# Optimization experiments

Hardware: AMD Instinct MI355X
Metric: run time of the kernel (lower is better)

Reference implementation:

```python
import jax, jax.numpy as jnp
import numpy as np

B, IN, HID, H = 8192, 1024, 2048, 8
UP = 2 * IN          # input_size * proj_factor
HS = HID // H        # head size = 256
EPS = 1e-5


def _blockdiag(x, w, b):
    # x: [B, UP] -> chunk into H blocks of UP//H, per-block linear to HID//H
    xb = x.reshape(B, H, UP // H)
    y = jnp.einsum('bhi,hio->bho', xb, w)
    return y.reshape(B, HID) + b


def setup_inputs() -> dict:
    key = jax.random.key(0)
    ks = jax.random.split(key, 20)
    rn = lambda k, s: jax.random.normal(k, s, jnp.float32)
    p = lambda k, *s: rn(k, s) * 0.02
    return dict(
        x=rn(ks[0], (B, IN)),
        h_prev=rn(ks[1], (B, HID)), c_prev=rn(ks[2], (B, HID)),
        n_prev=rn(ks[3], (B, HID)), m_prev=rn(ks[4], (B, HID)),
        ln_g=jnp.ones(IN), ln_b=jnp.zeros(IN),
        w_ul=p(ks[5], IN, UP), b_ul=jnp.zeros(UP),
        w_ur=p(ks[6], IN, HID), b_ur=jnp.zeros(HID),
        conv_w=p(ks[7], 4), conv_b=jnp.zeros(()),
        w_skip=p(ks[8], UP, HID), b_skip=jnp.zeros(HID),
        w_q=p(ks[9], H, UP // H, HID // H), b_q=jnp.zeros(HID),
        w_k=p(ks[10], H, UP // H, HID // H), b_k=jnp.zeros(HID),
        w_v=p(ks[11], H, UP // H, HID // H), b_v=jnp.zeros(HID),
        w_i=p(ks[12], UP, HID), b_i=jnp.zeros(HID),
        w_f=p(ks[13], UP, HID), b_f=jnp.zeros(HID),
        w_o=p(ks[14], UP, HID), b_o=jnp.zeros(HID),
        gn_g=jnp.ones(HID), gn_b=jnp.zeros(HID),
        w_down=p(ks[15], HID, IN), b_down=jnp.zeros(IN),
    )


def reference(x, h_prev, c_prev, n_prev, m_prev, ln_g, ln_b,
              w_ul, b_ul, w_ur, b_ur, conv_w, conv_b, w_skip, b_skip,
              w_q, b_q, w_k, b_k, w_v, b_v, w_i, b_i, w_f, b_f, w_o, b_o,
              gn_g, gn_b, w_down, b_down):
    # LayerNorm over features
    mu = x.mean(-1, keepdims=True)
    var = x.var(-1, keepdims=True)
    xn = (x - mu) * jax.lax.rsqrt(var + EPS) * ln_g + ln_b

    xul = xn @ w_ul + b_ul          # [B, UP]
    xur = xn @ w_ur + b_ur          # [B, HID]

    # causal conv1d (kernel 4, 1 channel) along the feature axis, left-pad 3
    xp = jnp.pad(xul, ((0, 0), (3, 0)))
    xc = conv_b + sum(conv_w[j] * xp[:, j:j + UP] for j in range(4))
    xc = jax.nn.silu(xc)            # [B, UP]

    x_skip = xc @ w_skip + b_skip

    q = _blockdiag(xc, w_q, b_q)
    k = _blockdiag(xc, w_k, b_k) / np.sqrt(HS).astype(np.float32)
    v = _blockdiag(xul, w_v, b_v)

    i_t = xc @ w_i + b_i
    f_t = xc @ w_f + b_f
    o = jax.nn.sigmoid(xul @ w_o + b_o)

    m_t = jnp.maximum(f_t + m_prev, i_t)
    i = jnp.exp(i_t - m_t)
    f = jnp.exp(f_t + m_prev - m_t)
    c_t = f * c_prev + i * (v * k)
    n_t = f * n_prev + i * k

    denom = jnp.max(jnp.abs(n_t.T @ q), axis=1)     # [HID]
    h_t = o * (c_t * q) / denom

    # GroupNorm on (N, C), groups = H
    hg = h_t.reshape(B, H, HID // H)
    gm = hg.mean(-1, keepdims=True)
    gv = hg.var(-1, keepdims=True)
    hn = ((hg - gm) * jax.lax.rsqrt(gv + EPS)).reshape(B, HID) * gn_g + gn_b

    out = (hn + x_skip) * jax.nn.silu(xur)
    return out @ w_down + b_down + x, h_t, c_t, n_t, m_t
```

## Files before the change

kernel.cpp:

```cpp
#include <hip/hip_runtime.h>
#include <stdint.h>

#define B_    8192
#define IN_   1024
#define HID_  2048
#define UP_   2048
#define H_    8
#define HS_   256
#define EPS_  1e-5f

typedef __bf16 bf16x8 __attribute__((ext_vector_type(8)));
typedef float f32x4 __attribute__((ext_vector_type(4)));
typedef unsigned short u16x4 __attribute__((ext_vector_type(4)));
typedef unsigned short u16x8 __attribute__((ext_vector_type(8)));

__device__ __forceinline__ unsigned short f2bf(float f) {
  union { float f; unsigned int u; } v; v.f = f;
  unsigned int u = v.u;
  unsigned int r = (u + 0x7fffu + ((u >> 16) & 1u)) >> 16;
  return (unsigned short)r;
}
__device__ __forceinline__ float bf2f(unsigned short h) {
  union { unsigned int u; float f; } v; v.u = ((unsigned int)h) << 16;
  return v.f;
}

__device__ __forceinline__ void gload_lds16(const void* g, void* l) {
  auto gp = reinterpret_cast<const uint32_t __attribute__((address_space(1)))*>(
      reinterpret_cast<uintptr_t>(g));
  auto lp = reinterpret_cast<uint32_t __attribute__((address_space(3)))*>(
      reinterpret_cast<uintptr_t>(l));
  __builtin_amdgcn_global_load_lds(gp, lp, 16, 0, 0);
}

template <typename OutT, bool HAS_ADD>
__global__ __launch_bounds__(512, 2) void gemm8p(
    const unsigned short* __restrict__ A, int lda, int a_zoff,
    const unsigned short* __restrict__ W, int ldw, int w_zoff,
    const float* __restrict__ bias, const float* __restrict__ bias2,
    int bias_zoff,
    OutT* __restrict__ C, OutT* __restrict__ C2, int ldc, int c_zoff,
    int c_split,
    const float* __restrict__ ADD, float scale, float scale2, int K)
{
  __shared__ char lds[163840];
  const int z = blockIdx.z;
  A += (size_t)z * a_zoff;
  W += (size_t)z * w_zoff;
  if (bias) bias += (size_t)z * bias_zoff;
  if (bias2) bias2 += (size_t)z * bias_zoff;

  const int nwg = gridDim.x * gridDim.y;
  const int orig = blockIdx.y * gridDim.x + blockIdx.x;
  const int q8 = nwg >> 3, r8 = nwg & 7;
  const int xcd = orig & 7, xi = orig >> 3;
  const int wg = (xcd < r8 ? xcd * (q8 + 1) : r8 * (q8 + 1) + (xcd - r8) * q8) + xi;
  const int bx = wg % gridDim.x, by = wg / gridDim.x;

  const int t = threadIdx.x;
  const int lane = t & 63, wave = t >> 6;
  const int wr = wave >> 2, wc = wave & 3;
  const int l15 = lane & 15, l4 = lane >> 4;
  const int row0 = by * 256, col0 = bx * 256;

  const int lrow = lane >> 3;
  const int lslot = (lane & 7) ^ lrow;
  const size_t aLane = (size_t)lrow * lda * 2 + (size_t)lslot * 16;
  const size_t wLane = (size_t)lrow * ldw * 2 + (size_t)lslot * 16;
  const char* Abase = (const char*)A;
  const char* Wbase = (const char*)W;

  const int aRdBase = (wr * 128 + l15) * 128 + (((l4) ^ (l15 & 7)) * 16);
  const int bRdBase = (wc * 64 + l15) * 128 + (((l4) ^ (l15 & 7)) * 16);

  auto issueA = [&](int abuf, int half, int tile) {
#pragma unroll
    for (int j = 0; j < 2; ++j) {
      const int rbase = half * 128 + j * 64 + wave * 8;
      gload_lds16(Abase + (size_t)(row0 + rbase) * (lda * 2) + (size_t)tile * 128 + aLane,
                  lds + abuf * 32768 + rbase * 128 + lane * 16);
    }
  };
  auto issueB = [&](int bbuf, int half, int tile) {
#pragma unroll
    for (int j = 0; j < 2; ++j) {
      const int rbase = half * 128 + j * 64 + wave * 8;
      gload_lds16(Wbase + (size_t)(col0 + rbase) * (ldw * 2) + (size_t)tile * 128 + wLane,
                  lds + 98304 + bbuf * 32768 + rbase * 128 + lane * 16);
    }
  };

  f32x4 acc[8][4] = {};
  const int NT = K >> 6;

  issueA(0, 0, 0); issueA(0, 1, 0);
  issueB(0, 0, 0); issueB(0, 1, 0);
  if (NT > 1) {
    issueA(1, 0, 1); issueA(1, 1, 1);
    issueB(1, 0, 1); issueB(1, 1, 1);
    asm volatile("s_waitcnt vmcnt(8)" ::: "memory");
  } else {
    asm volatile("s_waitcnt vmcnt(0)" ::: "memory");
  }
  __builtin_amdgcn_s_barrier();
  __builtin_amdgcn_sched_barrier(0);

  for (int T = 0; T < NT; ++T) {
    const char* ldsA = lds + (T % 3) * 32768;
    const char* ldsB = lds + 98304 + (T & 1) * 32768;
    const int abufN = (T + 2) % 3;
    const int bbufN = T & 1;
    bf16x8 bfr[4][2];
#pragma unroll
    for (int q = 0; q < 4; ++q) {
      if (q == 0) {
#pragma unroll
        for (int ni = 0; ni < 4; ++ni) {
          bfr[ni][0] = *(const bf16x8*)(ldsB + (bRdBase + ni * 2048));
          bfr[ni][1] = *(const bf16x8*)(ldsB + ((bRdBase + ni * 2048) ^ 64));
        }
      }
      bf16x8 af[2][2];
#pragma unroll
      for (int m2 = 0; m2 < 2; ++m2) {
        const int mi = q * 2 + m2;
        af[m2][0] = *(const bf16x8*)(ldsA + (aRdBase + mi * 2048));
        af[m2][1] = *(const bf16x8*)(ldsA + ((aRdBase + mi * 2048) ^ 64));
      }
      if (q == 0 && T + 2 < NT) issueA(abufN, 0, T + 2);
      if (q == 1 && T + 2 < NT) issueA(abufN, 1, T + 2);
      if (q == 2 && T + 2 < NT) issueB(bbufN, 0, T + 2);
      if (q == 3 && T + 2 < NT) issueB(bbufN, 1, T + 2);
      if (q == 0) asm volatile("s_waitcnt lgkmcnt(8)" ::: "memory");
      __builtin_amdgcn_s_barrier();
      asm volatile("s_waitcnt lgkmcnt(0)" ::: "memory");
      __builtin_amdgcn_sched_barrier(0);
      __builtin_amdgcn_s_setprio(1);
#pragma unroll
      for (int kq = 0; kq < 2; ++kq)
#pragma unroll
        for (int m2 = 0; m2 < 2; ++m2)
#pragma unroll
          for (int ni = 0; ni < 4; ++ni)
            acc[q * 2 + m2][ni] = __builtin_amdgcn_mfma_f32_16x16x32_bf16(
                af[m2][kq], bfr[ni][kq], acc[q * 2 + m2][ni], 0, 0, 0);
      __builtin_amdgcn_s_setprio(0);
      if (q == 3) {
        if (T + 2 < NT) asm volatile("s_waitcnt vmcnt(8)" ::: "memory");
        else            asm volatile("s_waitcnt vmcnt(0)" ::: "memory");
      }
      __builtin_amdgcn_s_barrier();
      __builtin_amdgcn_sched_barrier(0);
    }
  }

  const float* bp = bias;
  OutT* Cp = C;
  int cbase = col0;
  float sc = scale;
  if (col0 >= c_split) { bp = bias2; Cp = C2; cbase = col0 - c_split; sc = scale2; }
#pragma unroll
  for (int mi = 0; mi < 8; ++mi) {
#pragma unroll
    for (int ni = 0; ni < 4; ++ni) {
#pragma unroll
      for (int r = 0; r < 4; ++r) {
        const int m = row0 + wr * 128 + mi * 16 + l4 * 4 + r;
        const int n = wc * 64 + ni * 16 + l15;
        float v = acc[mi][ni][r];
        if (bp) v += bp[cbase + n];
        v *= sc;
        const size_t ci = (size_t)m * ldc + (size_t)z * c_zoff + cbase + n;
        if constexpr (HAS_ADD) v += ADD[ci];
        if constexpr (sizeof(OutT) == 2) Cp[ci] = (OutT)f2bf(v);
        else Cp[ci] = v;
      }
    }
  }
}

__global__ __launch_bounds__(256) void denom_reduce(
    const float* __restrict__ part, float* __restrict__ denom)
{
  const int m = blockIdx.x, t = threadIdx.x;
  const size_t P = (size_t)HID_ * HID_;
  float v = 0.f;
  for (int n = t; n < HID_; n += 256) {
    const size_t o = (size_t)m * HID_ + n;
    float s = part[o] + part[P + o] + part[2 * P + o] + part[3 * P + o];
    v = fmaxf(v, fabsf(s));
  }
#pragma unroll
  for (int off = 1; off < 64; off <<= 1) v = fmaxf(v, __shfl_xor(v, off, 64));
  __shared__ float red[4];
  if ((t & 63) == 0) red[t >> 6] = v;
  __syncthreads();
  if (t == 0) denom[m] = fmaxf(fmaxf(red[0], red[1]), fmaxf(red[2], red[3]));
}

__global__ __launch_bounds__(256) void down_reduce(
    const float* __restrict__ part, const float* __restrict__ x,
    const float* __restrict__ bias, float* __restrict__ out)
{
  const size_t idx = ((size_t)blockIdx.x * 256 + threadIdx.x) * 4;
  const size_t P = (size_t)B_ * IN_;
  f32x4 a = *(const f32x4*)(part + idx);
  f32x4 b = *(const f32x4*)(part + P + idx);
  f32x4 xv = *(const f32x4*)(x + idx);
  const int j = (int)(idx & (IN_ - 1));
  f32x4 bv = *(const f32x4*)(bias + j);
  f32x4 o;
#pragma unroll
  for (int e = 0; e < 4; ++e) o[e] = a[e] + b[e] + bv[e] + xv[e];
  *(f32x4*)(out + idx) = o;
}

template <typename InT>
__global__ __launch_bounds__(256) void transpose_bf(
    const InT* __restrict__ in, unsigned short* __restrict__ out, int R, int C,
    int izoff, int ozoff)
{
  __shared__ float tile[32][33];
  in += (size_t)blockIdx.z * izoff;
  out += (size_t)blockIdx.z * ozoff;
  const int cb = blockIdx.x * 32, rb = blockIdx.y * 32;
  const int tx = threadIdx.x, ty = threadIdx.y;
  for (int i = ty; i < 32; i += 8) {
    InT v = in[(size_t)(rb + i) * C + cb + tx];
    float f;
    if constexpr (sizeof(InT) == 2) f = bf2f((unsigned short)v);
    else f = (float)v;
    tile[i][tx] = f;
  }
  __syncthreads();
  for (int i = ty; i < 32; i += 8)
    out[(size_t)(cb + i) * R + rb + tx] = f2bf(tile[tx][i]);
}

__global__ __launch_bounds__(256) void ln_kernel(
    const float* __restrict__ x, const float* __restrict__ g,
    const float* __restrict__ b, unsigned short* __restrict__ xn)
{
  const int brow = blockIdx.x, t = threadIdx.x;
  const int lane = t & 63, wave = t >> 6;
  const float* xr = x + (size_t)brow * IN_;
  f32x4 v = *(const f32x4*)(xr + t * 4);
  float s = v[0] + v[1] + v[2] + v[3];
  float q = v[0]*v[0] + v[1]*v[1] + v[2]*v[2] + v[3]*v[3];
#pragma unroll
  for (int off = 32; off; off >>= 1) {
    s += __shfl_xor(s, off, 64);
    q += __shfl_xor(q, off, 64);
  }
  __shared__ float ss[4], sq[4];
  if (lane == 0) { ss[wave] = s; sq[wave] = q; }
  __syncthreads();
  s = ss[0] + ss[1] + ss[2] + ss[3];
  q = sq[0] + sq[1] + sq[2] + sq[3];
  const float mean = s * (1.f / IN_);
  const float var = q * (1.f / IN_) - mean * mean;
  const float rs = rsqrtf(var + EPS_);
  u16x4 o;
#pragma unroll
  for (int e = 0; e < 4; ++e) {
    const int j = t * 4 + e;
    o[e] = f2bf((v[e] - mean) * rs * g[j] + b[j]);
  }
  *(u16x4*)(xn + (size_t)brow * IN_ + t * 4) = o;
}

__global__ __launch_bounds__(256) void conv_kernel(
    const unsigned short* __restrict__ xul, const float* __restrict__ cw,
    const float* __restrict__ cb, unsigned short* __restrict__ xc)
{
  const int brow = blockIdx.x, t = threadIdx.x;
  const size_t base = (size_t)brow * UP_;
  const int j0 = t * 8;
  float xv[11];
#pragma unroll
  for (int e = 0; e < 11; ++e) {
    const int j = j0 + e - 3;
    xv[e] = (j >= 0) ? bf2f(xul[base + j]) : 0.f;
  }
  const float w0 = cw[0], w1 = cw[1], w2 = cw[2], w3 = cw[3], bb = cb[0];
  u16x8 o;
#pragma unroll
  for (int e = 0; e < 8; ++e) {
    float sv = bb + w0 * xv[e] + w1 * xv[e + 1] + w2 * xv[e + 2] + w3 * xv[e + 3];
    o[e] = f2bf(sv / (1.f + expf(-sv)));
  }
  *(u16x8*)(xc + base + j0) = o;
}

__global__ __launch_bounds__(256) void gates_kernel(
    const unsigned short* __restrict__ sif,
    const unsigned short* __restrict__ kb, const unsigned short* __restrict__ vb,
    const float* __restrict__ mprev, const float* __restrict__ cprev,
    const float* __restrict__ nprev,
    float* __restrict__ mo, float* __restrict__ co, float* __restrict__ no,
    unsigned short* __restrict__ nT)
{
  __shared__ unsigned short nt_t[64][72];
  const int t = threadIdx.x;
  const int r = t >> 2, cq = t & 3;
  const int row = blockIdx.y * 64 + r;
  const int colb = blockIdx.x * 64 + cq * 16;
  const size_t hidb = (size_t)row * HID_ + colb;
  const size_t sifb = (size_t)row * 6144 + colb;
#pragma unroll
  for (int e4 = 0; e4 < 4; ++e4) {
    const int c4 = e4 * 4;
    f32x4 mp = *(const f32x4*)(mprev + hidb + c4);
    f32x4 cp = *(const f32x4*)(cprev + hidb + c4);
    f32x4 np = *(const f32x4*)(nprev + hidb + c4);
    u16x4 iv = *(const u16x4*)(sif + sifb + 2048 + c4);
    u16x4 fv = *(const u16x4*)(sif + sifb + 4096 + c4);
    u16x4 kv = *(const u16x4*)(kb + hidb + c4);
    u16x4 vv = *(const u16x4*)(vb + hidb + c4);
    f32x4 mo4, co4, no4;
#pragma unroll
    for (int e = 0; e < 4; ++e) {
      const float ft = bf2f(fv[e]) + mp[e];
      const float it = bf2f(iv[e]);
      const float mt = fmaxf(ft, it);
      const float ie = expf(it - mt);
      const float fe = expf(ft - mt);
      const float k = bf2f(kv[e]), v = bf2f(vv[e]);
      mo4[e] = mt;
      co4[e] = fe * cp[e] + ie * (v * k);
      no4[e] = fe * np[e] + ie * k;
      nt_t[r][cq * 16 + c4 + e] = f2bf(no4[e]);
    }
    *(f32x4*)(mo + hidb + c4) = mo4;
    *(f32x4*)(co + hidb + c4) = co4;
    *(f32x4*)(no + hidb + c4) = no4;
  }
  __syncthreads();
  const int cT = t >> 2, sq = t & 3;
  u16x8 o0, o1;
#pragma unroll
  for (int e = 0; e < 8; ++e) {
    o0[e] = nt_t[sq * 16 + e][cT];
    o1[e] = nt_t[sq * 16 + 8 + e][cT];
  }
  const size_t ob = (size_t)(blockIdx.x * 64 + cT) * B_ + blockIdx.y * 64 + sq * 16;
  *(u16x8*)(nT + ob) = o0;
  *(u16x8*)(nT + ob + 8) = o1;
}

__global__ __launch_bounds__(256) void hgn_kernel(
    const float* __restrict__ ct, const unsigned short* __restrict__ olin,
    const unsigned short* __restrict__ qb, const float* __restrict__ denom,
    const unsigned short* __restrict__ sif, const unsigned short* __restrict__ xurb,
    const float* __restrict__ gng, const float* __restrict__ gnb,
    float* __restrict__ ho, unsigned short* __restrict__ pre)
{
  const int brow = blockIdx.x, t = threadIdx.x;
  const size_t base = (size_t)brow * HID_ + t * 8;
  u16x8 ov = *(const u16x8*)(olin + base);
  u16x8 qv = *(const u16x8*)(qb + base);
  f32x4 c0 = *(const f32x4*)(ct + base);
  f32x4 c1 = *(const f32x4*)(ct + base + 4);
  float h[8];
  float s = 0.f, sq = 0.f;
#pragma unroll
  for (int e = 0; e < 8; ++e) {
    const float o = 1.f / (1.f + expf(-bf2f(ov[e])));
    const float cv = (e < 4) ? c0[e] : c1[e - 4];
    const float hv = o * cv * bf2f(qv[e]) / denom[t * 8 + e];
    h[e] = hv; s += hv; sq += hv * hv;
  }
#pragma unroll
  for (int e = 0; e < 8; ++e) ho[base + e] = h[e];
#pragma unroll
  for (int off = 1; off < 32; off <<= 1) {
    s += __shfl_xor(s, off, 64);
    sq += __shfl_xor(sq, off, 64);
  }
  const float mean = s * (1.f / HS_);
  const float var = sq * (1.f / HS_) - mean * mean;
  const float rs = rsqrtf(var + EPS_);
  u16x8 sv = *(const u16x8*)(sif + (size_t)brow * 6144 + t * 8);
  u16x8 xv = *(const u16x8*)(xurb + base);
  u16x8 pv;
#pragma unroll
  for (int e = 0; e < 8; ++e) {
    const int j = t * 8 + e;
    const float hn = (h[e] - mean) * rs * gng[j] + gnb[j];
    const float xr = bf2f(xv[e]);
    const float sil = xr / (1.f + expf(-xr));
    pv[e] = f2bf((hn + bf2f(sv[e])) * sil);
  }
  *(u16x8*)(pre + base) = pv;
}

extern "C" void kernel_launch(void* const* d_in, const int* in_sizes, int n_in,
                              void* d_out, int out_size, void* d_ws, size_t ws_size,
                              hipStream_t stream)
{
  const float* x      = (const float*)d_in[0];
  const float* c_prev = (const float*)d_in[2];
  const float* n_prev = (const float*)d_in[3];
  const float* m_prev = (const float*)d_in[4];
  const float* ln_g   = (const float*)d_in[5];
  const float* ln_b   = (const float*)d_in[6];
  const float* w_ul   = (const float*)d_in[7];
  const float* b_ul   = (const float*)d_in[8];
  const float* w_ur   = (const float*)d_in[9];
  const float* b_ur   = (const float*)d_in[10];
  const float* conv_w = (const float*)d_in[11];
  const float* conv_b = (const float*)d_in[12];
  const float* w_skip = (const float*)d_in[13];
  const float* b_skip = (const float*)d_in[14];
  const float* w_q    = (const float*)d_in[15];
  const float* b_q    = (const float*)d_in[16];
  const float* w_k    = (const float*)d_in[17];
  const float* b_k    = (const float*)d_in[18];
  const float* w_v    = (const float*)d_in[19];
  const float* b_v    = (const float*)d_in[20];
  const float* w_i    = (const float*)d_in[21];
  const float* b_i    = (const float*)d_in[22];
  const float* w_f    = (const float*)d_in[23];
  const float* b_f    = (const float*)d_in[24];
  const float* w_o    = (const float*)d_in[25];
  const float* b_o    = (const float*)d_in[26];
  const float* gn_g   = (const float*)d_in[27];
  const float* gn_b   = (const float*)d_in[28];
  const float* w_down = (const float*)d_in[29];
  const float* b_down = (const float*)d_in[30];

  float* out_p = (float*)d_out;
  float* h_p = out_p + (size_t)B_ * IN_;
  float* c_p = h_p + (size_t)B_ * HID_;
  float* n_p = c_p + (size_t)B_ * HID_;
  float* m_p = n_p + (size_t)B_ * HID_;

  char* ws = (char*)d_ws;
  size_t off = 0;
  auto alloc = [&](size_t n) -> void* {
    void* p = ws + off;
    off += (n + 255) & ~(size_t)255;
    return p;
  };

  const size_t BH2 = (size_t)B_ * HID_ * 2;

  unsigned short* xn_bf   = (unsigned short*)alloc((size_t)B_ * IN_ * 2);
  unsigned short* xul_bf  = (unsigned short*)alloc(BH2);
  unsigned short* xur_bf  = (unsigned short*)alloc(BH2);
  unsigned short* xc_bf   = (unsigned short*)alloc(BH2);
  unsigned short* sif_bf  = (unsigned short*)alloc((size_t)B_ * 6144 * 2);
  unsigned short* q_bf    = (unsigned short*)alloc(BH2);
  unsigned short* k_bf    = (unsigned short*)alloc(BH2);
  unsigned short* v_bf    = (unsigned short*)alloc(BH2);
  unsigned short* olin_bf = (unsigned short*)alloc(BH2);
  unsigned short* qT_bf   = (unsigned short*)alloc(BH2);
  unsigned short* nT_bf   = (unsigned short*)alloc(BH2);
  unsigned short* pre_bf  = (unsigned short*)alloc(BH2);
  float* denom = (float*)alloc(HID_ * sizeof(float));
  float* part  = (float*)alloc((size_t)4 * HID_ * HID_ * sizeof(float));
  float* b_sif = (float*)alloc(6144 * sizeof(float));
  unsigned short* wt_ulur = (unsigned short*)alloc((size_t)4096 * IN_ * 2);
  unsigned short* wt_sif  = (unsigned short*)alloc((size_t)6144 * UP_ * 2);
  unsigned short* wt_qk   = (unsigned short*)alloc((size_t)H_ * 512 * HS_ * 2);
  unsigned short* wt_v    = (unsigned short*)alloc((size_t)H_ * HS_ * HS_ * 2);
  unsigned short* wt_o    = (unsigned short*)alloc((size_t)UP_ * HID_ * 2);
  unsigned short* wt_down = (unsigned short*)alloc((size_t)HID_ * IN_ * 2);

  if (off > ws_size) return;

  const dim3 tb32(32, 8);
  const int NOSPLIT = 1 << 30;

  hipMemcpyAsync(b_sif, b_skip, 2048 * 4, hipMemcpyDeviceToDevice, stream);
  hipMemcpyAsync(b_sif + 2048, b_i, 2048 * 4, hipMemcpyDeviceToDevice, stream);
  hipMemcpyAsync(b_sif + 4096, b_f, 2048 * 4, hipMemcpyDeviceToDevice, stream);

  transpose_bf<float><<<dim3(64, 32, 1), tb32, 0, stream>>>(w_ul, wt_ulur, 1024, 2048, 0, 0);
  transpose_bf<float><<<dim3(64, 32, 1), tb32, 0, stream>>>(w_ur, wt_ulur + (size_t)2048 * 1024, 1024, 2048, 0, 0);
  transpose_bf<float><<<dim3(64, 64, 1), tb32, 0, stream>>>(w_skip, wt_sif, 2048, 2048, 0, 0);
  transpose_bf<float><<<dim3(64, 64, 1), tb32, 0, stream>>>(w_i, wt_sif + (size_t)2048 * 2048, 2048, 2048, 0, 0);
  transpose_bf<float><<<dim3(64, 64, 1), tb32, 0, stream>>>(w_f, wt_sif + (size_t)4096 * 2048, 2048, 2048, 0, 0);
  transpose_bf<float><<<dim3(8, 8, 8), tb32, 0, stream>>>(w_q, wt_qk, 256, 256, 65536, 131072);
  transpose_bf<float><<<dim3(8, 8, 8), tb32, 0, stream>>>(w_k, wt_qk + 65536, 256, 256, 65536, 131072);
  transpose_bf<float><<<dim3(8, 8, 8), tb32, 0, stream>>>(w_v, wt_v, 256, 256, 65536, 65536);
  transpose_bf<float><<<dim3(64, 64, 1), tb32, 0, stream>>>(w_o, wt_o, 2048, 2048, 0, 0);
  transpose_bf<float><<<dim3(32, 64, 1), tb32, 0, stream>>>(w_down, wt_down, 2048, 1024, 0, 0);

  ln_kernel<<<B_, 256, 0, stream>>>(x, ln_g, ln_b, xn_bf);

  gemm8p<unsigned short, false><<<dim3(16, 32, 1), 512, 0, stream>>>(
      xn_bf, IN_, 0, wt_ulur, IN_, 0, b_ul, b_ur, 0,
      xul_bf, xur_bf, HID_, 0, 2048, nullptr, 1.f, 1.f, IN_);

  conv_kernel<<<B_, 256, 0, stream>>>(xul_bf, conv_w, conv_b, xc_bf);

  gemm8p<unsigned short, false><<<dim3(24, 32, 1), 512, 0, stream>>>(
      xc_bf, UP_, 0, wt_sif, UP_, 0, b_sif, nullptr, 0,
      sif_bf, sif_bf, 6144, 0, NOSPLIT, nullptr, 1.f, 1.f, UP_);

  gemm8p<unsigned short, false><<<dim3(2, 32, 8), 512, 0, stream>>>(
      xc_bf, UP_, HS_, wt_qk, HS_, 512 * HS_, b_q, b_k, HS_,
      q_bf, k_bf, HID_, HS_, 256, nullptr, 1.f, 0.0625f, HS_);

  gemm8p<unsigned short, false><<<dim3(1, 32, 8), 512, 0, stream>>>(
      xul_bf, UP_, HS_, wt_v, HS_, HS_ * HS_, b_v, nullptr, HS_,
      v_bf, v_bf, HID_, HS_, NOSPLIT, nullptr, 1.f, 1.f, HS_);

  gemm8p<unsigned short, false><<<dim3(8, 32, 1), 512, 0, stream>>>(
      xul_bf, UP_, 0, wt_o, UP_, 0, b_o, nullptr, 0,
      olin_bf, olin_bf, HID_, 0, NOSPLIT, nullptr, 1.f, 1.f, UP_);

  gates_kernel<<<dim3(HID_ / 64, B_ / 64, 1), 256, 0, stream>>>(
      sif_bf, k_bf, v_bf, m_prev, c_prev, n_prev, m_p, c_p, n_p, nT_bf);

  transpose_bf<unsigned short><<<dim3(64, 256, 1), tb32, 0, stream>>>(
      q_bf, qT_bf, B_, HID_, 0, 0);

  gemm8p<float, false><<<dim3(8, 8, 4), 512, 0, stream>>>(
      nT_bf, B_, B_ / 4, qT_bf, B_, B_ / 4, nullptr, nullptr, 0,
      part, part, HID_, HID_ * HID_, NOSPLIT, nullptr, 1.f, 1.f, B_ / 4);
  denom_reduce<<<HID_, 256, 0, stream>>>(part, denom);

  hgn_kernel<<<B_, 256, 0, stream>>>(
      c_p, olin_bf, q_bf, denom, sif_bf, xur_bf, gn_g, gn_b, h_p, pre_bf);

  gemm8p<float, false><<<dim3(4, 32, 2), 512, 0, stream>>>(
      pre_bf, UP_, 1024, wt_down, UP_, 1024, nullptr, nullptr, 0,
      part, part, IN_, B_ * IN_, NOSPLIT, nullptr, 1.f, 1.f, 1024);
  down_reduce<<<(B_ * IN_ / 4) / 256, 256, 0, stream>>>(part, x, b_down, out_p);
}
```

Baseline: 1.005 ms.

## Double-buffer A fragments in registers to overlap LDS reads with MFMA

Software-pipelines the LDS reads of the A-operand fragments in the GEMM main loop. Each quarter-step now runs its MFMA cluster on fragments loaded one step earlier, alternating between two register sets, and the last quarter prefetches the next K-tile's first fragments. The global-to-LDS issue, the vmcnt wait (now vmcnt(6)) and the barrier are moved ahead of the LDS reads so the next buffer is ready before it is prefetched. The aim is to hide LDS latency behind matrix math, at the cost of extra VGPRs under a 512-thread, 2-blocks-per-CU launch bound, which could cause spills.

```diff
diff --git a/kernel.cpp b/kernel.cpp
--- a/kernel.cpp
+++ b/kernel.cpp
@@ -32,6 +32,22 @@
       reinterpret_cast<uintptr_t>(l));
   __builtin_amdgcn_global_load_lds(gp, lp, 16, 0, 0);
 }
+
+#define PREFETCH_AF(DST, BASE, MI0)                                         \
+  DST[0][0] = *(const bf16x8*)((BASE) + (aRdBase + (MI0) * 2048));          \
+  DST[0][1] = *(const bf16x8*)((BASE) + ((aRdBase + (MI0) * 2048) ^ 64));   \
+  DST[1][0] = *(const bf16x8*)((BASE) + (aRdBase + ((MI0) + 1) * 2048));    \
+  DST[1][1] = *(const bf16x8*)((BASE) + ((aRdBase + ((MI0) + 1) * 2048) ^ 64));
+
+#define MFMA_CLUSTER(AF, Q)                                                 \
+  _Pragma("unroll")                                                         \
+  for (int kq = 0; kq < 2; ++kq)                                            \
+    _Pragma("unroll")                                                       \
+    for (int m2 = 0; m2 < 2; ++m2)                                          \
+      _Pragma("unroll")                                                     \
+      for (int ni = 0; ni < 4; ++ni)                                        \
+        acc[(Q) * 2 + m2][ni] = __builtin_amdgcn_mfma_f32_16x16x32_bf16(    \
+            AF[m2][kq], bfr[ni][kq], acc[(Q) * 2 + m2][ni], 0, 0, 0);
 
 template <typename OutT, bool HAS_ADD>
 __global__ __launch_bounds__(512, 2) void gemm8p(
@@ -93,6 +109,9 @@
   f32x4 acc[8][4] = {};
   const int NT = K >> 6;
 
+  bf16x8 bfr[4][2];
+  bf16x8 afA[2][2], afB[2][2];
+
   issueA(0, 0, 0); issueA(0, 1, 0);
   issueB(0, 0, 0); issueB(0, 1, 0);
   if (NT > 1) {
@@ -104,15 +123,28 @@
   }
   __builtin_amdgcn_s_barrier();
   __builtin_amdgcn_sched_barrier(0);
+  {
+    const char* ldsA0 = lds;
+    PREFETCH_AF(afA, ldsA0, 0)
+  }
 
   for (int T = 0; T < NT; ++T) {
     const char* ldsA = lds + (T % 3) * 32768;
+    const char* ldsAn = lds + ((T + 1) % 3) * 32768;
     const char* ldsB = lds + 98304 + (T & 1) * 32768;
     const int abufN = (T + 2) % 3;
     const int bbufN = T & 1;
-    bf16x8 bfr[4][2];
 #pragma unroll
     for (int q = 0; q < 4; ++q) {
+      if (q == 3) {
+        if (T + 2 < NT) asm volatile("s_waitcnt vmcnt(6)" ::: "memory");
+        else            asm volatile("s_waitcnt vmcnt(0)" ::: "memory");
+      }
+      if (q == 0 && T + 2 < NT) issueA(abufN, 0, T + 2);
+      if (q == 1 && T + 2 < NT) issueA(abufN, 1, T + 2);
+      if (q == 2 && T + 2 < NT) issueB(bbufN, 0, T + 2);
+      if (q == 3 && T + 2 < NT) issueB(bbufN, 1, T + 2);
+      __builtin_amdgcn_s_barrier();
       if (q == 0) {
 #pragma unroll
         for (int ni = 0; ni < 4; ++ni) {
@@ -120,35 +152,16 @@
           bfr[ni][1] = *(const bf16x8*)(ldsB + ((bRdBase + ni * 2048) ^ 64));
         }
       }
-      bf16x8 af[2][2];
-#pragma unroll
-      for (int m2 = 0; m2 < 2; ++m2) {
-        const int mi = q * 2 + m2;
-        af[m2][0] = *(const bf16x8*)(ldsA + (aRdBase + mi * 2048));
-        af[m2][1] = *(const bf16x8*)(ldsA + ((aRdBase + mi * 2048) ^ 64));
-      }
-      if (q == 0 && T + 2 < NT) issueA(abufN, 0, T + 2);
-      if (q == 1 && T + 2 < NT) issueA(abufN, 1, T + 2);
-      if (q == 2 && T + 2 < NT) issueB(bbufN, 0, T + 2);
-      if (q == 3 && T + 2 < NT) issueB(bbufN, 1, T + 2);
-      if (q == 0) asm volatile("s_waitcnt lgkmcnt(8)" ::: "memory");
-      __builtin_amdgcn_s_barrier();
       asm volatile("s_waitcnt lgkmcnt(0)" ::: "memory");
       __builtin_amdgcn_sched_barrier(0);
+      if (q == 0) { PREFETCH_AF(afB, ldsA, 2) }
+      else if (q == 1) { PREFETCH_AF(afA, ldsA, 4) }
+      else if (q == 2) { PREFETCH_AF(afB, ldsA, 6) }
+      else if (T + 1 < NT) { PREFETCH_AF(afA, ldsAn, 0) }
       __builtin_amdgcn_s_setprio(1);
-#pragma unroll
-      for (int kq = 0; kq < 2; ++kq)
-#pragma unroll
-        for (int m2 = 0; m2 < 2; ++m2)
-#pragma unroll
-          for (int ni = 0; ni < 4; ++ni)
-            acc[q * 2 + m2][ni] = __builtin_amdgcn_mfma_f32_16x16x32_bf16(
-                af[m2][kq], bfr[ni][kq], acc[q * 2 + m2][ni], 0, 0, 0);
+      if ((q & 1) == 0) { MFMA_CLUSTER(afA, q) }
+      else              { MFMA_CLUSTER(afB, q) }
       __builtin_amdgcn_s_setprio(0);
-      if (q == 3) {
-        if (T + 2 < NT) asm volatile("s_waitcnt vmcnt(8)" ::: "memory");
-        else            asm volatile("s_waitcnt vmcnt(0)" ::: "memory");
-      }
       __builtin_amdgcn_s_barrier();
       __builtin_amdgcn_sched_barrier(0);
     }
```

After: 1.026 ms. 1.02x slower.
